# Kernel optimization log

Hardware: AMD Instinct MI355X
Metric: run time of the kernel (lower is better)

## Reference

```python
import jax, jax.numpy as jnp
import numpy as np

N_NODES = 100000
N_EDGES = 1600000
D_IN, D_HID, D_OUT = 64, 128, 64


def setup_inputs() -> dict:
    key = jax.random.key(0)
    ks = jax.random.split(key, 12)
    s = lambda d: 1.0 / np.sqrt(d)
    return {
        "x": jax.random.normal(ks[0], (N_NODES, D_IN), dtype=jnp.float32),
        "edge_index": jax.random.randint(ks[1], (2, N_EDGES), 0, N_NODES, dtype=jnp.int64),
        # conv1 MLP: Linear(D_IN->D_HID), ReLU, Linear(D_HID->D_HID)
        "W1a": jax.random.uniform(ks[2], (D_IN, D_HID), jnp.float32, -s(D_IN), s(D_IN)),
        "b1a": jnp.zeros((D_HID,), jnp.float32),
        "W1b": jax.random.uniform(ks[3], (D_HID, D_HID), jnp.float32, -s(D_HID), s(D_HID)),
        "b1b": jnp.zeros((D_HID,), jnp.float32),
        # conv2 MLP: Linear(D_HID->D_HID), ReLU, Linear(D_HID->D_HID)
        "W2a": jax.random.uniform(ks[4], (D_HID, D_HID), jnp.float32, -s(D_HID), s(D_HID)),
        "b2a": jnp.zeros((D_HID,), jnp.float32),
        "W2b": jax.random.uniform(ks[5], (D_HID, D_HID), jnp.float32, -s(D_HID), s(D_HID)),
        "b2b": jnp.zeros((D_HID,), jnp.float32),
        # final projection Linear(D_HID->D_OUT)
        "Wlin": jax.random.uniform(ks[6], (D_HID, D_OUT), jnp.float32, -s(D_HID), s(D_HID)),
        "blin": jnp.zeros((D_OUT,), jnp.float32),
    }


def _gin_conv(h, src, dst, Wa, ba, Wb, bb, num_nodes):
    # GINConv (eps=0): MLP((1+eps)*x + sum_{j->i} x_j)
    agg = jax.ops.segment_sum(h[src], dst, num_segments=num_nodes)  # [N, d]
    z = h + agg
    z = jax.nn.relu(z @ Wa + ba)
    return z @ Wb + bb


def reference(x, edge_index, W1a, b1a, W1b, b1b, W2a, b2a, W2b, b2b, Wlin, blin):
    n = x.shape[0]
    src, dst = edge_index[0], edge_index[1]
    h = jax.nn.relu(_gin_conv(x, src, dst, W1a, b1a, W1b, b1b, n))
    h = jax.nn.relu(_gin_conv(h, src, dst, W2a, b2a, W2b, b2b, n))
    return h @ Wlin + blin  # [N, D_OUT]
```

## Files before the change

### kernel.cpp

```cpp
#include <hip/hip_runtime.h>
#include <hip/hip_fp16.h>


typedef __attribute__((ext_vector_type(8))) short short8;
typedef __attribute__((ext_vector_type(4))) float f32x4;
union F8 { unsigned u[4]; short8 s; };

__device__ inline unsigned bfpair(float v) {
    unsigned u = __float_as_uint(v);
    unsigned rh = u + 0x7fffu + ((u >> 16) & 1u);
    unsigned hf = rh & 0xffff0000u;
    float lof = v - __uint_as_float(hf);
    unsigned ul = __float_as_uint(lof);
    unsigned rl = ul + 0x7fffu + ((ul >> 16) & 1u);
    return (rh >> 16) | (rl & 0xffff0000u);
}


constexpr int BUCKET_SHIFT = 9;
constexpr int BUCKET_NODES = 1 << BUCKET_SHIFT;
constexpr int CAP = 10240;
constexpr int EPB = 4096;
constexpr int NBUCK_MAX = 256;

__global__ __launch_bounds__(256) void init_gcur_kernel(int* __restrict__ gcur, int nbuck) {
    int i = threadIdx.x;
    if (i < nbuck) gcur[i] = i * CAP;
}

__global__ __launch_bounds__(256) void bucket_scatter_kernel(const int* __restrict__ ei, int E,
                                                             int* __restrict__ gcur,
                                                             int* __restrict__ gpk,
                                                             int nbuck) {
    __shared__ int spk[EPB];
    __shared__ unsigned char sbuck[EPB];
    __shared__ int lcnt[NBUCK_MAX];
    __shared__ int lbase[NBUCK_MAX];
    __shared__ int lcur[NBUCK_MAX];
    __shared__ int gbase[NBUCK_MAX];
    __shared__ int stmp[256];

    const int t = threadIdx.x;
    const int e0 = blockIdx.x * EPB;
    const int ecnt = min(EPB, E - e0);

    for (int i = t; i < NBUCK_MAX; i += 256) lcnt[i] = 0;
    __syncthreads();

    for (int i = t; i < ecnt; i += 256) {
        int d = ei[E + e0 + i];
        atomicAdd(&lcnt[d >> BUCKET_SHIFT], 1);
    }
    __syncthreads();

    int v = lcnt[t];
    stmp[t] = v;
    __syncthreads();
    #pragma unroll
    for (int off = 1; off < 256; off <<= 1) {
        int add = (t >= off) ? stmp[t - off] : 0;
        __syncthreads();
        stmp[t] += add;
        __syncthreads();
    }
    lbase[t] = stmp[t] - v;
    lcur[t] = stmp[t] - v;
    __syncthreads();

    for (int i = t; i < ecnt; i += 256) {
        int s = ei[e0 + i];
        int d = ei[E + e0 + i];
        int b = d >> BUCKET_SHIFT;
        int p = atomicAdd(&lcur[b], 1);
        spk[p] = ((d & (BUCKET_NODES - 1)) << 17) | s;
        sbuck[p] = (unsigned char)b;
    }
    __syncthreads();

    if (t < nbuck) {
        int c = lcnt[t];
        gbase[t] = (c > 0) ? atomicAdd(&gcur[t], c) : 0;
    }
    __syncthreads();

    for (int i = t; i < ecnt; i += 256) {
        int b = sbuck[i];
        int gp = gbase[b] + (i - lbase[b]);
        if (gp < (b + 1) * CAP) gpk[gp] = spk[i];
    }
}

__global__ __launch_bounds__(256) void bucket_hist_kernel(const int* __restrict__ gpk,
                                                          const int* __restrict__ gcur,
                                                          int* __restrict__ cnt, int N) {
    __shared__ int h[BUCKET_NODES];
    const int t = threadIdx.x;
    const int b = blockIdx.x;
    const int base = b << BUCKET_SHIFT;
    for (int i = t; i < BUCKET_NODES; i += 256) h[i] = 0;
    __syncthreads();
    int cb = min(gcur[b] - b * CAP, CAP);
    const int* pp = gpk + (size_t)b * CAP;
    for (int i = t; i < cb; i += 256) atomicAdd(&h[((unsigned)pp[i]) >> 17], 1);
    __syncthreads();
    for (int i = t; i < BUCKET_NODES && base + i < N; i += 256) cnt[base + i] = h[i];
}

__global__ __launch_bounds__(256) void scan_block_kernel(const int* __restrict__ cnt,
                                                         int* __restrict__ rs,
                                                         int* __restrict__ partials,
                                                         int N) {
    __shared__ int s[256];
    int t = threadIdx.x;
    int i = blockIdx.x * 256 + t;
    int v = (i < N) ? cnt[i] : 0;
    s[t] = v;
    __syncthreads();
    #pragma unroll
    for (int off = 1; off < 256; off <<= 1) {
        int add = (t >= off) ? s[t - off] : 0;
        __syncthreads();
        s[t] += add;
        __syncthreads();
    }
    if (i < N) rs[i] = s[t] - v;
    if (t == 255) partials[blockIdx.x] = s[255];
}

__global__ __launch_bounds__(512) void scan_partials_kernel(int* __restrict__ partials,
                                                            int nb) {
    __shared__ int s[512];
    int t = threadIdx.x;
    int v = (t < nb) ? partials[t] : 0;
    s[t] = v;
    __syncthreads();
    #pragma unroll
    for (int off = 1; off < 512; off <<= 1) {
        int add = (t >= off) ? s[t - off] : 0;
        __syncthreads();
        s[t] += add;
        __syncthreads();
    }
    if (t < nb) partials[t] = s[t] - v;
}

__global__ __launch_bounds__(256) void scan_add_kernel(int* __restrict__ rs,
                                                       const int* __restrict__ partials,
                                                       int N, int E) {
    int i = blockIdx.x * 256 + threadIdx.x;
    if (i < N) rs[i] += partials[blockIdx.x];
    if (i == 0) rs[N] = E;
}

__global__ __launch_bounds__(256) void bucket_fill_kernel(const int* __restrict__ gpk,
                                                          const int* __restrict__ gcur,
                                                          const int* __restrict__ rs,
                                                          int* __restrict__ edge_src, int N) {
    __shared__ int cur[BUCKET_NODES];
    const int t = threadIdx.x;
    const int b = blockIdx.x;
    const int base = b << BUCKET_SHIFT;
    for (int i = t; i < BUCKET_NODES; i += 256) cur[i] = rs[min(base + i, N)];
    __syncthreads();
    int cb = min(gcur[b] - b * CAP, CAP);
    const int* pp = gpk + (size_t)b * CAP;
    for (int i = t; i < cb; i += 256) {
        unsigned pw = (unsigned)pp[i];
        int p = atomicAdd(&cur[pw >> 17], 1);
        edge_src[p] = (int)(pw & 0x1FFFFu);
    }
}


__global__ __launch_bounds__(256) void convert_fp16_kernel(const float* __restrict__ src,
                                                           __half2* __restrict__ dst, int n2) {
    int i = blockIdx.x * 256 + threadIdx.x;
    if (i < n2) {
        float2 v = reinterpret_cast<const float2*>(src)[i];
        dst[i] = __floats2half2_rn(v.x, v.y);
    }
}

__global__ __launch_bounds__(256) void agg128_fp16(const __half2* __restrict__ H16,
                                                   const int* __restrict__ row_start,
                                                   const int* __restrict__ edge_src,
                                                   __half2* __restrict__ Z16, int N) {
    int wave = threadIdx.x >> 6, lane = threadIdx.x & 63;
    int node = blockIdx.x * 4 + wave;
    if (node >= N) return;
    int beg = row_start[node], end = row_start[node + 1];
    float2 self = __half22float2(H16[(size_t)node * 64 + lane]);
    float a0 = self.x, a1 = self.y;
    int i = beg;
    for (; i + 8 <= end; i += 8) {
        int s[8];
        #pragma unroll
        for (int j = 0; j < 8; ++j) s[j] = edge_src[i + j];
        float2 v[8];
        #pragma unroll
        for (int j = 0; j < 8; ++j) v[j] = __half22float2(H16[(size_t)s[j] * 64 + lane]);
        #pragma unroll
        for (int j = 0; j < 8; ++j) { a0 += v[j].x; a1 += v[j].y; }
    }
    for (; i < end; ++i) {
        float2 v = __half22float2(H16[(size_t)edge_src[i] * 64 + lane]);
        a0 += v.x;
        a1 += v.y;
    }
    Z16[(size_t)node * 64 + lane] = __floats2half2_rn(a0, a1);
}

__global__ __launch_bounds__(256) void agg64_fp16(const __half2* __restrict__ H16,
                                                  const int* __restrict__ row_start,
                                                  const int* __restrict__ edge_src,
                                                  __half2* __restrict__ Z16, int N) {
    int t = threadIdx.x;
    int grp = t >> 5;
    int gl = t & 31;
    int node = blockIdx.x * 8 + grp;
    if (node >= N) return;
    int beg = row_start[node], end = row_start[node + 1];
    float2 self = __half22float2(H16[(size_t)node * 32 + gl]);
    float a0 = self.x, a1 = self.y;
    int i = beg;
    for (; i + 8 <= end; i += 8) {
        int s[8];
        #pragma unroll
        for (int j = 0; j < 8; ++j) s[j] = edge_src[i + j];
        float2 v[8];
        #pragma unroll
        for (int j = 0; j < 8; ++j) v[j] = __half22float2(H16[(size_t)s[j] * 32 + gl]);
        #pragma unroll
        for (int j = 0; j < 8; ++j) { a0 += v[j].x; a1 += v[j].y; }
    }
    for (; i < end; ++i) {
        float2 v = __half22float2(H16[(size_t)edge_src[i] * 32 + gl]);
        a0 += v.x;
        a1 += v.y;
    }
    Z16[(size_t)node * 32 + gl] = __floats2half2_rn(a0, a1);
}


__global__ __launch_bounds__(256) void prep_weights_kernel(const float* __restrict__ W1a,
                                                           const float* __restrict__ W1b,
                                                           const float* __restrict__ W2a,
                                                           const float* __restrict__ W2b,
                                                           const float* __restrict__ Wlin,
                                                           short* __restrict__ hi,
                                                           short* __restrict__ lo) {
    int i = blockIdx.x * 256 + threadIdx.x;
    const float* W;
    int base, K, N;
    if (i < 8192)       { W = W1a;  base = 0;     K = 64;  N = 128; }
    else if (i < 24576) { W = W1b;  base = 8192;  K = 128; N = 128; }
    else if (i < 40960) { W = W2a;  base = 24576; K = 128; N = 128; }
    else if (i < 57344) { W = W2b;  base = 40960; K = 128; N = 128; }
    else                { W = Wlin; base = 57344; K = 128; N = 64;  }
    int rel = i - base;
    int NT = N >> 4;
    int j  = rel & 7;
    int l  = (rel >> 3) & 63;
    int tc = rel >> 9;
    int nt = tc % NT;
    int c  = tc / NT;
    int n  = nt * 16 + (l & 15);
    int k  = c * 32 + ((l >> 4) << 3) + j;
    float v = W[k * N + n];
    unsigned p = bfpair(v);
    hi[i] = (short)(p & 0xffffu);
    lo[i] = (short)(p >> 16);
}


template <int K>
__device__ inline void stage_global16(const __half2* __restrict__ z, int M, int m0,
                                      unsigned* __restrict__ P, int t) {
    constexpr int KC = K / 32;
    constexpr int NF = 8 * KC * 64;
    #pragma unroll
    for (int fi = t; fi < NF; fi += 256) {
        int l = fi & 63;
        int tc = fi >> 6;
        int c = tc & (KC - 1);
        int T = tc / KC;
        int row = m0 + T * 16 + (l & 15);
        if (row >= M) row = M - 1;
        int kb = c * 32 + ((l >> 4) << 3);
        const __half2* p = z + (size_t)row * (K / 2) + (kb >> 1);
        uint4 v = *reinterpret_cast<const uint4*>(p);
        float2 f0 = __half22float2(*reinterpret_cast<__half2*>(&v.x));
        float2 f1 = __half22float2(*reinterpret_cast<__half2*>(&v.y));
        float2 f2 = __half22float2(*reinterpret_cast<__half2*>(&v.z));
        float2 f3 = __half22float2(*reinterpret_cast<__half2*>(&v.w));
        int base = ((T * KC + c) * 8) * 66 + l;
        P[base + 0 * 66] = bfpair(f0.x);
        P[base + 1 * 66] = bfpair(f0.y);
        P[base + 2 * 66] = bfpair(f1.x);
        P[base + 3 * 66] = bfpair(f1.y);
        P[base + 4 * 66] = bfpair(f2.x);
        P[base + 5 * 66] = bfpair(f2.y);
        P[base + 6 * 66] = bfpair(f3.x);
        P[base + 7 * 66] = bfpair(f3.y);
    }
}

template <int K, int NT>
__device__ inline void stage_compute(const unsigned* __restrict__ P,
                                     const short* __restrict__ WH,
                                     const short* __restrict__ WL,
                                     int w, int lane, f32x4 (*acc)[8]) {
    constexpr int KC = K / 32;
    const short8* bhp = reinterpret_cast<const short8*>(WH) + lane;
    const short8* blp = reinterpret_cast<const short8*>(WL) + lane;
    for (int c = 0; c < KC; ++c) {
        F8 bh[NT], bl[NT];
        #pragma unroll
        for (int nt = 0; nt < NT; ++nt) {
            bh[nt].s = bhp[(c * NT + nt) * 64];
            bl[nt].s = blp[(c * NT + nt) * 64];
        }
        #pragma unroll
        for (int mt = 0; mt < 2; ++mt) {
            const int T = w * 2 + mt;
            const unsigned* Pb = P + ((T * KC + c) * 8) * 66 + lane;
            unsigned d[8];
            #pragma unroll
            for (int j = 0; j < 8; ++j) d[j] = Pb[j * 66];
            F8 ah, al;
            #pragma unroll
            for (int j = 0; j < 4; ++j) {
                ah.u[j] = __builtin_amdgcn_perm(d[2 * j + 1], d[2 * j], 0x05040100u);
                al.u[j] = __builtin_amdgcn_perm(d[2 * j + 1], d[2 * j], 0x07060302u);
            }
            #pragma unroll
            for (int nt = 0; nt < NT; ++nt) {
                acc[mt][nt] = __builtin_amdgcn_mfma_f32_16x16x32_bf16(ah.s, bh[nt].s, acc[mt][nt], 0, 0, 0);
                acc[mt][nt] = __builtin_amdgcn_mfma_f32_16x16x32_bf16(al.s, bh[nt].s, acc[mt][nt], 0, 0, 0);
                acc[mt][nt] = __builtin_amdgcn_mfma_f32_16x16x32_bf16(ah.s, bl[nt].s, acc[mt][nt], 0, 0, 0);
            }
        }
    }
}

__device__ inline void epilogue_tile(const f32x4* acc, const float* __restrict__ bias,
                                     unsigned* __restrict__ Pout, int T, int lane) {
    int q = lane >> 4, ln = lane & 15;
    #pragma unroll
    for (int nt = 0; nt < 8; ++nt) {
        int col = nt * 16 + ln;
        float b = bias[col];
        int c = col >> 5, jj = col & 7, q2 = (col >> 3) & 3;
        int pb = ((T * 4 + c) * 8 + jj) * 66;
        #pragma unroll
        for (int r = 0; r < 4; ++r) {
            float v = fmaxf(acc[nt][r] + b, 0.f);
            Pout[pb + ((q * 4 + r) | (q2 << 4))] = bfpair(v);
        }
    }
}

__global__ __launch_bounds__(256, 2) void mfma_mlp_A(const __half2* __restrict__ z16,
                                                     const short* __restrict__ WaH,
                                                     const short* __restrict__ WaL,
                                                     const float* __restrict__ ba,
                                                     const short* __restrict__ WbH,
                                                     const short* __restrict__ WbL,
                                                     const float* __restrict__ bb,
                                                     __half* __restrict__ H16out, int M) {
    __shared__ unsigned P[8 * 4 * 8 * 66];
    const int t = threadIdx.x;
    const int w = t >> 6, lane = t & 63;
    const int m0 = blockIdx.x * 128;
    const int q = lane >> 4, ln = lane & 15;

    stage_global16<64>(z16, M, m0, P, t);
    __syncthreads();

    f32x4 acc[2][8];
    #pragma unroll
    for (int mt = 0; mt < 2; ++mt)
        #pragma unroll
        for (int i = 0; i < 8; ++i) acc[mt][i] = (f32x4){0.f, 0.f, 0.f, 0.f};
    stage_compute<64, 8>(P, WaH, WaL, w, lane, acc);
    __syncthreads();
    epilogue_tile(acc[0], ba, P, w * 2 + 0, lane);
    epilogue_tile(acc[1], ba, P, w * 2 + 1, lane);
    __syncthreads();

    #pragma unroll
    for (int mt = 0; mt < 2; ++mt)
        #pragma unroll
        for (int i = 0; i < 8; ++i) acc[mt][i] = (f32x4){0.f, 0.f, 0.f, 0.f};
    stage_compute<128, 8>(P, WbH, WbL, w, lane, acc);

    #pragma unroll
    for (int mt = 0; mt < 2; ++mt) {
        #pragma unroll
        for (int nt = 0; nt < 8; ++nt) {
            int col = nt * 16 + ln;
            float b = bb[col];
            #pragma unroll
            for (int r = 0; r < 4; ++r) {
                int row = m0 + (w * 2 + mt) * 16 + q * 4 + r;
                if (row < M) {
                    float v = fmaxf(acc[mt][nt][r] + b, 0.f);
                    H16out[(size_t)row * 128 + col] = __float2half_rn(v);
                }
            }
        }
    }
}

__global__ __launch_bounds__(256, 2) void mfma_mlp_B(const __half2* __restrict__ z16,
                                                     const short* __restrict__ WaH,
                                                     const short* __restrict__ WaL,
                                                     const float* __restrict__ ba,
                                                     const short* __restrict__ WbH,
                                                     const short* __restrict__ WbL,
                                                     const float* __restrict__ bb,
                                                     const short* __restrict__ WlH,
                                                     const short* __restrict__ WlL,
                                                     const float* __restrict__ bl,
                                                     float* __restrict__ Out, int M) {
    __shared__ unsigned P[8 * 4 * 8 * 66];
    const int t = threadIdx.x;
    const int w = t >> 6, lane = t & 63;
    const int m0 = blockIdx.x * 128;
    const int q = lane >> 4, ln = lane & 15;

    stage_global16<128>(z16, M, m0, P, t);
    __syncthreads();

    f32x4 acc[2][8];
    #pragma unroll
    for (int mt = 0; mt < 2; ++mt)
        #pragma unroll
        for (int i = 0; i < 8; ++i) acc[mt][i] = (f32x4){0.f, 0.f, 0.f, 0.f};
    stage_compute<128, 8>(P, WaH, WaL, w, lane, acc);
    __syncthreads();
    epilogue_tile(acc[0], ba, P, w * 2 + 0, lane);
    epilogue_tile(acc[1], ba, P, w * 2 + 1, lane);
    __syncthreads();

    #pragma unroll
    for (int mt = 0; mt < 2; ++mt)
        #pragma unroll
        for (int i = 0; i < 8; ++i) acc[mt][i] = (f32x4){0.f, 0.f, 0.f, 0.f};
    stage_compute<128, 8>(P, WbH, WbL, w, lane, acc);
    __syncthreads();
    epilogue_tile(acc[0], bb, P, w * 2 + 0, lane);
    epilogue_tile(acc[1], bb, P, w * 2 + 1, lane);
    __syncthreads();

    #pragma unroll
    for (int mt = 0; mt < 2; ++mt)
        #pragma unroll
        for (int i = 0; i < 8; ++i) acc[mt][i] = (f32x4){0.f, 0.f, 0.f, 0.f};
    stage_compute<128, 4>(P, WlH, WlL, w, lane, acc);

    #pragma unroll
    for (int mt = 0; mt < 2; ++mt) {
        #pragma unroll
        for (int nt = 0; nt < 4; ++nt) {
            int col = nt * 16 + ln;
            float b = bl[col];
            #pragma unroll
            for (int r = 0; r < 4; ++r) {
                int row = m0 + (w * 2 + mt) * 16 + q * 4 + r;
                if (row < M) Out[(size_t)row * 64 + col] = acc[mt][nt][r] + b;
            }
        }
    }
}


extern "C" void kernel_launch(void* const* d_in, const int* in_sizes, int n_in,
                              void* d_out, int out_size, void* d_ws, size_t ws_size,
                              hipStream_t stream) {
    const float* x    = (const float*)d_in[0];
    const int*   ei   = (const int*)d_in[1];
    const float* W1a  = (const float*)d_in[2];
    const float* b1a  = (const float*)d_in[3];
    const float* W1b  = (const float*)d_in[4];
    const float* b1b  = (const float*)d_in[5];
    const float* W2a  = (const float*)d_in[6];
    const float* b2a  = (const float*)d_in[7];
    const float* W2b  = (const float*)d_in[8];
    const float* b2b  = (const float*)d_in[9];
    const float* Wlin = (const float*)d_in[10];
    const float* blin = (const float*)d_in[11];
    float* out = (float*)d_out;

    const int N = in_sizes[0] / 64;
    const int E = in_sizes[1] / 2;
    const int NBUCK = (N + BUCKET_NODES - 1) >> BUCKET_SHIFT;

    char* ws = (char*)d_ws;
    const size_t bufBytes = (size_t)N * 128 * sizeof(float);
    __half2* Zbuf = (__half2*)(ws + 0);
    char* B = ws + bufBytes;
    size_t off = 3 * bufBytes;
    int* row_start = (int*)(ws + off); off += ((size_t)(N + 1) * 4 + 15) & ~(size_t)15;
    int* cnt       = (int*)(ws + off); off += ((size_t)N * 4 + 15) & ~(size_t)15;
    int* partials  = (int*)(ws + off); off += 4096;
    int* gcur      = (int*)(ws + off); off += 4096;
    int* edge_src  = (int*)(ws + off); off += (size_t)E * 4;
    __half* h116   = (__half*)(ws + off); off += (size_t)N * 128 * 2;
    int* gpk = (int*)B;
    short* wHi = (short*)(B + (32u << 20));
    short* wLo = wHi + 65536;
    __half* x16 = (__half*)(B + (36u << 20));
    short* w1aH = wHi + 0;     short* w1aL = wLo + 0;
    short* w1bH = wHi + 8192;  short* w1bL = wLo + 8192;
    short* w2aH = wHi + 24576; short* w2aL = wLo + 24576;
    short* w2bH = wHi + 40960; short* w2bL = wLo + 40960;
    short* wlH  = wHi + 57344; short* wlL  = wLo + 57344;

    const int NB_N = (N + 255) / 256;
    const int NB_G = (N + 127) / 128;
    const int NB_S = (E + EPB - 1) / EPB;
    const int NB_A128 = (N + 3) / 4;
    const int NB_A64  = (N + 7) / 8;
    const int NB_CVT  = (N * 64 / 2 + 255) / 256;

    prep_weights_kernel<<<256, 256, 0, stream>>>(W1a, W1b, W2a, W2b, Wlin, wHi, wLo);
    convert_fp16_kernel<<<NB_CVT, 256, 0, stream>>>(x, (__half2*)x16, N * 32);

    init_gcur_kernel<<<1, 256, 0, stream>>>(gcur, NBUCK);
    bucket_scatter_kernel<<<NB_S, 256, 0, stream>>>(ei, E, gcur, gpk, NBUCK);
    bucket_hist_kernel<<<NBUCK, 256, 0, stream>>>(gpk, gcur, cnt, N);
    scan_block_kernel<<<NB_N, 256, 0, stream>>>(cnt, row_start, partials, N);
    scan_partials_kernel<<<1, 512, 0, stream>>>(partials, NB_N);
    scan_add_kernel<<<NB_N, 256, 0, stream>>>(row_start, partials, N, E);
    bucket_fill_kernel<<<NBUCK, 256, 0, stream>>>(gpk, gcur, row_start, edge_src, N);

    agg64_fp16<<<NB_A64, 256, 0, stream>>>((const __half2*)x16, row_start, edge_src, Zbuf, N);
    mfma_mlp_A<<<NB_G, 256, 0, stream>>>(Zbuf, w1aH, w1aL, b1a, w1bH, w1bL, b1b, h116, N);

    agg128_fp16<<<NB_A128, 256, 0, stream>>>((const __half2*)h116, row_start, edge_src, Zbuf, N);
    mfma_mlp_B<<<NB_G, 256, 0, stream>>>(Zbuf, w2aH, w2aL, b2a, w2bH, w2bL, b2b,
                                         wlH, wlL, blin, out, N);
}
```

Baseline: 370.9 us.

## Fuse neighbor aggregation into MFMA MLP kernels and merge prep kernels

The gather-sum aggregation now runs inside the MLP kernels: each block aggregates its 128 nodes and writes bf16 hi/lo pairs straight into the shared-memory operand tile. This removes the intermediate fp16 Z buffer round-trip to global memory and two kernel launches. Weight prep, x conversion and gcur init are merged into one prep kernel. In exchange the gather now runs in MLP blocks limited to two per CU with one wave per row serially, so it has less parallelism and fewer loads in flight to hide gather latency.

```diff
diff --git a/kernel.cpp b/kernel.cpp
--- a/kernel.cpp
+++ b/kernel.cpp
@@ -22,11 +22,6 @@
 constexpr int CAP = 10240;
 constexpr int EPB = 4096;
 constexpr int NBUCK_MAX = 256;
-
-__global__ __launch_bounds__(256) void init_gcur_kernel(int* __restrict__ gcur, int nbuck) {
-    int i = threadIdx.x;
-    if (i < nbuck) gcur[i] = i * CAP;
-}
 
 __global__ __launch_bounds__(256) void bucket_scatter_kernel(const int* __restrict__ ei, int E,
                                                              int* __restrict__ gcur,
@@ -172,138 +167,121 @@
 }
 
 
-__global__ __launch_bounds__(256) void convert_fp16_kernel(const float* __restrict__ src,
-                                                           __half2* __restrict__ dst, int n2) {
+__global__ __launch_bounds__(256) void prep_kernel(const float* __restrict__ W1a,
+                                                   const float* __restrict__ W1b,
+                                                   const float* __restrict__ W2a,
+                                                   const float* __restrict__ W2b,
+                                                   const float* __restrict__ Wlin,
+                                                   short* __restrict__ hi,
+                                                   short* __restrict__ lo,
+                                                   const float* __restrict__ x,
+                                                   __half2* __restrict__ x16, int n2,
+                                                   int* __restrict__ gcur, int nbuck) {
     int i = blockIdx.x * 256 + threadIdx.x;
-    if (i < n2) {
-        float2 v = reinterpret_cast<const float2*>(src)[i];
-        dst[i] = __floats2half2_rn(v.x, v.y);
-    }
-}
-
-__global__ __launch_bounds__(256) void agg128_fp16(const __half2* __restrict__ H16,
-                                                   const int* __restrict__ row_start,
-                                                   const int* __restrict__ edge_src,
-                                                   __half2* __restrict__ Z16, int N) {
-    int wave = threadIdx.x >> 6, lane = threadIdx.x & 63;
-    int node = blockIdx.x * 4 + wave;
-    if (node >= N) return;
-    int beg = row_start[node], end = row_start[node + 1];
-    float2 self = __half22float2(H16[(size_t)node * 64 + lane]);
-    float a0 = self.x, a1 = self.y;
-    int i = beg;
-    for (; i + 8 <= end; i += 8) {
-        int s[8];
-        #pragma unroll
-        for (int j = 0; j < 8; ++j) s[j] = edge_src[i + j];
-        float2 v[8];
-        #pragma unroll
-        for (int j = 0; j < 8; ++j) v[j] = __half22float2(H16[(size_t)s[j] * 64 + lane]);
-        #pragma unroll
-        for (int j = 0; j < 8; ++j) { a0 += v[j].x; a1 += v[j].y; }
-    }
-    for (; i < end; ++i) {
-        float2 v = __half22float2(H16[(size_t)edge_src[i] * 64 + lane]);
-        a0 += v.x;
-        a1 += v.y;
-    }
-    Z16[(size_t)node * 64 + lane] = __floats2half2_rn(a0, a1);
-}
-
-__global__ __launch_bounds__(256) void agg64_fp16(const __half2* __restrict__ H16,
-                                                  const int* __restrict__ row_start,
-                                                  const int* __restrict__ edge_src,
-                                                  __half2* __restrict__ Z16, int N) {
-    int t = threadIdx.x;
-    int grp = t >> 5;
-    int gl = t & 31;
-    int node = blockIdx.x * 8 + grp;
-    if (node >= N) return;
-    int beg = row_start[node], end = row_start[node + 1];
-    float2 self = __half22float2(H16[(size_t)node * 32 + gl]);
-    float a0 = self.x, a1 = self.y;
-    int i = beg;
-    for (; i + 8 <= end; i += 8) {
-        int s[8];
-        #pragma unroll
-        for (int j = 0; j < 8; ++j) s[j] = edge_src[i + j];
-        float2 v[8];
-        #pragma unroll
-        for (int j = 0; j < 8; ++j) v[j] = __half22float2(H16[(size_t)s[j] * 32 + gl]);
-        #pragma unroll
-        for (int j = 0; j < 8; ++j) { a0 += v[j].x; a1 += v[j].y; }
-    }
-    for (; i < end; ++i) {
-        float2 v = __half22float2(H16[(size_t)edge_src[i] * 32 + gl]);
-        a0 += v.x;
-        a1 += v.y;
-    }
-    Z16[(size_t)node * 32 + gl] = __floats2half2_rn(a0, a1);
-}
-
-
-__global__ __launch_bounds__(256) void prep_weights_kernel(const float* __restrict__ W1a,
-                                                           const float* __restrict__ W1b,
-                                                           const float* __restrict__ W2a,
-                                                           const float* __restrict__ W2b,
-                                                           const float* __restrict__ Wlin,
-                                                           short* __restrict__ hi,
-                                                           short* __restrict__ lo) {
-    int i = blockIdx.x * 256 + threadIdx.x;
-    const float* W;
-    int base, K, N;
-    if (i < 8192)       { W = W1a;  base = 0;     K = 64;  N = 128; }
-    else if (i < 24576) { W = W1b;  base = 8192;  K = 128; N = 128; }
-    else if (i < 40960) { W = W2a;  base = 24576; K = 128; N = 128; }
-    else if (i < 57344) { W = W2b;  base = 40960; K = 128; N = 128; }
-    else                { W = Wlin; base = 57344; K = 128; N = 64;  }
-    int rel = i - base;
-    int NT = N >> 4;
-    int j  = rel & 7;
-    int l  = (rel >> 3) & 63;
-    int tc = rel >> 9;
-    int nt = tc % NT;
-    int c  = tc / NT;
-    int n  = nt * 16 + (l & 15);
-    int k  = c * 32 + ((l >> 4) << 3) + j;
-    float v = W[k * N + n];
-    unsigned p = bfpair(v);
-    hi[i] = (short)(p & 0xffffu);
-    lo[i] = (short)(p >> 16);
-}
-
-
-template <int K>
-__device__ inline void stage_global16(const __half2* __restrict__ z, int M, int m0,
-                                      unsigned* __restrict__ P, int t) {
-    constexpr int KC = K / 32;
-    constexpr int NF = 8 * KC * 64;
-    #pragma unroll
-    for (int fi = t; fi < NF; fi += 256) {
-        int l = fi & 63;
-        int tc = fi >> 6;
-        int c = tc & (KC - 1);
-        int T = tc / KC;
-        int row = m0 + T * 16 + (l & 15);
-        if (row >= M) row = M - 1;
-        int kb = c * 32 + ((l >> 4) << 3);
-        const __half2* p = z + (size_t)row * (K / 2) + (kb >> 1);
-        uint4 v = *reinterpret_cast<const uint4*>(p);
-        float2 f0 = __half22float2(*reinterpret_cast<__half2*>(&v.x));
-        float2 f1 = __half22float2(*reinterpret_cast<__half2*>(&v.y));
-        float2 f2 = __half22float2(*reinterpret_cast<__half2*>(&v.z));
-        float2 f3 = __half22float2(*reinterpret_cast<__half2*>(&v.w));
-        int base = ((T * KC + c) * 8) * 66 + l;
-        P[base + 0 * 66] = bfpair(f0.x);
-        P[base + 1 * 66] = bfpair(f0.y);
-        P[base + 2 * 66] = bfpair(f1.x);
-        P[base + 3 * 66] = bfpair(f1.y);
-        P[base + 4 * 66] = bfpair(f2.x);
-        P[base + 5 * 66] = bfpair(f2.y);
-        P[base + 6 * 66] = bfpair(f3.x);
-        P[base + 7 * 66] = bfpair(f3.y);
-    }
-}
+    if (blockIdx.x == 0 && threadIdx.x < nbuck) gcur[threadIdx.x] = threadIdx.x * CAP;
+    if (i < 65536) {
+        const float* W;
+        int base, K, N;
+        if (i < 8192)       { W = W1a;  base = 0;     K = 64;  N = 128; }
+        else if (i < 24576) { W = W1b;  base = 8192;  K = 128; N = 128; }
+        else if (i < 40960) { W = W2a;  base = 24576; K = 128; N = 128; }
+        else if (i < 57344) { W = W2b;  base = 40960; K = 128; N = 128; }
+        else                { W = Wlin; base = 57344; K = 128; N = 64;  }
+        int rel = i - base;
+        int NT = N >> 4;
+        int j  = rel & 7;
+        int l  = (rel >> 3) & 63;
+        int tc = rel >> 9;
+        int nt = tc % NT;
+        int c  = tc / NT;
+        int n  = nt * 16 + (l & 15);
+        int k  = c * 32 + ((l >> 4) << 3) + j;
+        float v = W[k * N + n];
+        unsigned p = bfpair(v);
+        hi[i] = (short)(p & 0xffffu);
+        lo[i] = (short)(p >> 16);
+    }
+    for (int k = i; k < n2; k += gridDim.x * 256) {
+        float2 v = reinterpret_cast<const float2*>(x)[k];
+        x16[k] = __floats2half2_rn(v.x, v.y);
+    }
+}
+
+
+__device__ inline void stage_agg128(const __half2* __restrict__ H16,
+                                    const int* __restrict__ row_start,
+                                    const int* __restrict__ edge_src,
+                                    int M, int m0, unsigned* __restrict__ P,
+                                    int w, int lane) {
+    const int c  = lane >> 4;
+    const int j0 = 2 * (lane & 3);
+    const int q2 = (lane >> 2) & 3;
+    for (int r = w * 32; r < w * 32 + 32; ++r) {
+        int node = m0 + r;
+        if (node >= M) break;
+        int beg = row_start[node], end = row_start[node + 1];
+        float2 self = __half22float2(H16[(size_t)node * 64 + lane]);
+        float a0 = self.x, a1 = self.y;
+        int i = beg;
+        for (; i + 8 <= end; i += 8) {
+            int s[8];
+            #pragma unroll
+            for (int j = 0; j < 8; ++j) s[j] = edge_src[i + j];
+            float2 v[8];
+            #pragma unroll
+            for (int j = 0; j < 8; ++j) v[j] = __half22float2(H16[(size_t)s[j] * 64 + lane]);
+            #pragma unroll
+            for (int j = 0; j < 8; ++j) { a0 += v[j].x; a1 += v[j].y; }
+        }
+        for (; i < end; ++i) {
+            float2 v = __half22float2(H16[(size_t)edge_src[i] * 64 + lane]);
+            a0 += v.x; a1 += v.y;
+        }
+        int pb = (((r >> 4) * 4 + c) * 8 + j0) * 66 + ((q2 << 4) | (r & 15));
+        P[pb]      = bfpair(a0);
+        P[pb + 66] = bfpair(a1);
+    }
+}
+
+__device__ inline void stage_agg64(const __half2* __restrict__ H16,
+                                   const int* __restrict__ row_start,
+                                   const int* __restrict__ edge_src,
+                                   int M, int m0, unsigned* __restrict__ P,
+                                   int w, int lane) {
+    const int sub = lane >> 5;
+    const int cl  = lane & 31;
+    const int c   = cl >> 4;
+    const int j0  = 2 * (cl & 3);
+    const int q2  = (cl >> 2) & 3;
+    for (int rp = w * 32; rp < w * 32 + 32; rp += 2) {
+        int r = rp + sub;
+        int node = m0 + r;
+        if (node < M) {
+            int beg = row_start[node], end = row_start[node + 1];
+            float2 self = __half22float2(H16[(size_t)node * 32 + cl]);
+            float a0 = self.x, a1 = self.y;
+            int i = beg;
+            for (; i + 8 <= end; i += 8) {
+                int s[8];
+                #pragma unroll
+                for (int j = 0; j < 8; ++j) s[j] = edge_src[i + j];
+                float2 v[8];
+                #pragma unroll
+                for (int j = 0; j < 8; ++j) v[j] = __half22float2(H16[(size_t)s[j] * 32 + cl]);
+                #pragma unroll
+                for (int j = 0; j < 8; ++j) { a0 += v[j].x; a1 += v[j].y; }
+            }
+            for (; i < end; ++i) {
+                float2 v = __half22float2(H16[(size_t)edge_src[i] * 32 + cl]);
+                a0 += v.x; a1 += v.y;
+            }
+            int pb = (((r >> 4) * 2 + c) * 8 + j0) * 66 + ((q2 << 4) | (r & 15));
+            P[pb]      = bfpair(a0);
+            P[pb + 66] = bfpair(a1);
+        }
+    }
+}
+
 
 template <int K, int NT>
 __device__ inline void stage_compute(const unsigned* __restrict__ P,
@@ -360,21 +338,23 @@
     }
 }
 
-__global__ __launch_bounds__(256, 2) void mfma_mlp_A(const __half2* __restrict__ z16,
-                                                     const short* __restrict__ WaH,
-                                                     const short* __restrict__ WaL,
-                                                     const float* __restrict__ ba,
-                                                     const short* __restrict__ WbH,
-                                                     const short* __restrict__ WbL,
-                                                     const float* __restrict__ bb,
-                                                     __half* __restrict__ H16out, int M) {
+__global__ __launch_bounds__(256, 2) void fused_mlp_A(const __half2* __restrict__ x16,
+                                                      const int* __restrict__ row_start,
+                                                      const int* __restrict__ edge_src,
+                                                      const short* __restrict__ WaH,
+                                                      const short* __restrict__ WaL,
+                                                      const float* __restrict__ ba,
+                                                      const short* __restrict__ WbH,
+                                                      const short* __restrict__ WbL,
+                                                      const float* __restrict__ bb,
+                                                      __half* __restrict__ H16out, int M) {
     __shared__ unsigned P[8 * 4 * 8 * 66];
     const int t = threadIdx.x;
     const int w = t >> 6, lane = t & 63;
     const int m0 = blockIdx.x * 128;
     const int q = lane >> 4, ln = lane & 15;
 
-    stage_global16<64>(z16, M, m0, P, t);
+    stage_agg64(x16, row_start, edge_src, M, m0, P, w, lane);
     __syncthreads();
 
     f32x4 acc[2][8];
@@ -412,24 +392,26 @@
     }
 }
 
-__global__ __launch_bounds__(256, 2) void mfma_mlp_B(const __half2* __restrict__ z16,
-                                                     const short* __restrict__ WaH,
-                                                     const short* __restrict__ WaL,
-                                                     const float* __restrict__ ba,
-                                                     const short* __restrict__ WbH,
-                                                     const short* __restrict__ WbL,
-                                                     const float* __restrict__ bb,
-                                                     const short* __restrict__ WlH,
-                                                     const short* __restrict__ WlL,
-                                                     const float* __restrict__ bl,
-                                                     float* __restrict__ Out, int M) {
+__global__ __launch_bounds__(256, 2) void fused_mlp_B(const __half2* __restrict__ h116,
+                                                      const int* __restrict__ row_start,
+                                                      const int* __restrict__ edge_src,
+                                                      const short* __restrict__ WaH,
+                                                      const short* __restrict__ WaL,
+                                                      const float* __restrict__ ba,
+                                                      const short* __restrict__ WbH,
+                                                      const short* __restrict__ WbL,
+                                                      const float* __restrict__ bb,
+                                                      const short* __restrict__ WlH,
+                                                      const short* __restrict__ WlL,
+                                                      const float* __restrict__ bl,
+                                                      float* __restrict__ Out, int M) {
     __shared__ unsigned P[8 * 4 * 8 * 66];
     const int t = threadIdx.x;
     const int w = t >> 6, lane = t & 63;
     const int m0 = blockIdx.x * 128;
     const int q = lane >> 4, ln = lane & 15;
 
-    stage_global16<128>(z16, M, m0, P, t);
+    stage_agg128(h116, row_start, edge_src, M, m0, P, w, lane);
     __syncthreads();
 
     f32x4 acc[2][8];
@@ -498,7 +480,6 @@
 
     char* ws = (char*)d_ws;
     const size_t bufBytes = (size_t)N * 128 * sizeof(float);
-    __half2* Zbuf = (__half2*)(ws + 0);
     char* B = ws + bufBytes;
     size_t off = 3 * bufBytes;
     int* row_start = (int*)(ws + off); off += ((size_t)(N + 1) * 4 + 15) & ~(size_t)15;
@@ -520,14 +501,11 @@
     const int NB_N = (N + 255) / 256;
     const int NB_G = (N + 127) / 128;
     const int NB_S = (E + EPB - 1) / EPB;
-    const int NB_A128 = (N + 3) / 4;
-    const int NB_A64  = (N + 7) / 8;
-    const int NB_CVT  = (N * 64 / 2 + 255) / 256;
-
-    prep_weights_kernel<<<256, 256, 0, stream>>>(W1a, W1b, W2a, W2b, Wlin, wHi, wLo);
-    convert_fp16_kernel<<<NB_CVT, 256, 0, stream>>>(x, (__half2*)x16, N * 32);
-
-    init_gcur_kernel<<<1, 256, 0, stream>>>(gcur, NBUCK);
+    const int NB_P = 12500;
+
+    prep_kernel<<<NB_P, 256, 0, stream>>>(W1a, W1b, W2a, W2b, Wlin, wHi, wLo,
+                                          x, (__half2*)x16, N * 32, gcur, NBUCK);
+
     bucket_scatter_kernel<<<NB_S, 256, 0, stream>>>(ei, E, gcur, gpk, NBUCK);
     bucket_hist_kernel<<<NBUCK, 256, 0, stream>>>(gpk, gcur, cnt, N);
     scan_block_kernel<<<NB_N, 256, 0, stream>>>(cnt, row_start, partials, N);
@@ -535,10 +513,10 @@
     scan_add_kernel<<<NB_N, 256, 0, stream>>>(row_start, partials, N, E);
     bucket_fill_kernel<<<NBUCK, 256, 0, stream>>>(gpk, gcur, row_start, edge_src, N);
 
-    agg64_fp16<<<NB_A64, 256, 0, stream>>>((const __half2*)x16, row_start, edge_src, Zbuf, N);
-    mfma_mlp_A<<<NB_G, 256, 0, stream>>>(Zbuf, w1aH, w1aL, b1a, w1bH, w1bL, b1b, h116, N);
-
-    agg128_fp16<<<NB_A128, 256, 0, stream>>>((const __half2*)h116, row_start, edge_src, Zbuf, N);
-    mfma_mlp_B<<<NB_G, 256, 0, stream>>>(Zbuf, w2aH, w2aL, b2a, w2bH, w2bL, b2b,
-                                         wlH, wlL, blin, out, N);
-}
+    fused_mlp_A<<<NB_G, 256, 0, stream>>>((const __half2*)x16, row_start, edge_src,
+                                          w1aH, w1aL, b1a, w1bH, w1bL, b1b, h116, N);
+
+    fused_mlp_B<<<NB_G, 256, 0, stream>>>((const __half2*)h116, row_start, edge_src,
+                                          w2aH, w2aL, b2a, w2bH, w2bL, b2b,
+                                          wlH, wlL, blin, out, N);
+}
```

After: 579.9 us. 56.4% more time.
